# Optimization experiments

Measured on AMD Instinct MI355X. Metric: run time of the kernel, lower is better.

The kernel has to match this reference:

```python
import math
import jax, jax.numpy as jnp
import numpy as np

NH, NKV, HD, THETA = 32, 8, 128, 500000.0

def rotate_half(x):
    x1, x2 = jnp.split(x, 2, axis=-1)
    return jnp.concatenate((-x2, x1), axis=-1)

def rope_cos_sin(seq_len, dim, base, dtype):
    inv_freq = 1.0 / (base ** (jnp.arange(0, dim, 2, dtype=jnp.float32) / dim))
    t = jnp.arange(seq_len, dtype=jnp.float32)
    freqs = jnp.outer(t, inv_freq)              # [S, dim/2]
    emb = jnp.concatenate((freqs, freqs), -1)   # [S, dim]
    return jnp.cos(emb).astype(dtype), jnp.sin(emb).astype(dtype)

def setup_inputs() -> dict:
    key = jax.random.key(0)
    ks = jax.random.split(key, 5)
    B, S, H = 1, 2048, 4096
    sc = 1.0 / math.sqrt(H)
    return {
        'x':  jax.random.normal(ks[0], (B, S, H), jnp.float32),
        'wq': jax.random.normal(ks[1], (H, H), jnp.float32) * sc,
        'wk': jax.random.normal(ks[2], (NKV * HD, H), jnp.float32) * sc,
        'wv': jax.random.normal(ks[3], (NKV * HD, H), jnp.float32) * sc,
        'wo': jax.random.normal(ks[4], (H, H), jnp.float32) * sc,
    }

def attention(x, wq, wk, wv, wo):
    B, S, H = x.shape
    n_rep = NH // NKV
    q = (x @ wq.T).reshape(B, S, NH, HD).transpose(0, 2, 1, 3)    # [B,NH,S,HD]
    k = (x @ wk.T).reshape(B, S, NKV, HD).transpose(0, 2, 1, 3)   # [B,NKV,S,HD]
    v = (x @ wv.T).reshape(B, S, NKV, HD).transpose(0, 2, 1, 3)
    cos, sin = rope_cos_sin(S, HD, THETA, x.dtype)                # [S,HD]
    cos = cos[None, None]; sin = sin[None, None]
    q = q * cos + rotate_half(q) * sin
    k = k * cos + rotate_half(k) * sin
    k = jnp.repeat(k, n_rep, axis=1)                               # [B,NH,S,HD]
    v = jnp.repeat(v, n_rep, axis=1)
    scores = jnp.einsum('bhqd,bhkd->bhqk', q, k) / math.sqrt(HD)
    causal = jnp.tril(jnp.ones((S, S), dtype=bool))
    scores = jnp.where(causal, scores, jnp.finfo(scores.dtype).min)
    probs = jax.nn.softmax(scores, axis=-1)
    out = jnp.einsum('bhqk,bhkd->bhqd', probs, v)                  # [B,NH,S,HD]
    out = out.transpose(0, 2, 1, 3).reshape(B, S, H)
    return out @ wo.T

def reference(x, wq, wk, wv, wo):
    return attention(x, wq, wk, wv, wo)
```

## Files before the change

kernel.cpp:

```cpp
#include <hip/hip_runtime.h>
#include <hip/hip_bf16.h>
#include <math.h>

typedef __bf16 bf16x8 __attribute__((ext_vector_type(8)));
typedef __bf16 bf16x4 __attribute__((ext_vector_type(4)));
typedef unsigned short u16x8 __attribute__((ext_vector_type(8)));
typedef float  f32x4  __attribute__((ext_vector_type(4)));

constexpr int kS   = 2048;
constexpr int kH   = 4096;
constexpr int kNH  = 32;
constexpr int kNKV = 8;
constexpr int kHD  = 128;
constexpr int kQKV = kH + 2 * kNKV * kHD;
constexpr int kKOff = kH;
constexpr int kVOff = kH + kNKV * kHD;

__global__ void cast_bf16(const float* __restrict__ in, __bf16* __restrict__ out, int n4) {
    int i = blockIdx.x * blockDim.x + threadIdx.x;
    if (i < n4) {
        float4 f = ((const float4*)in)[i];
        bf16x4 o;
        o[0] = (__bf16)f.x; o[1] = (__bf16)f.y; o[2] = (__bf16)f.z; o[3] = (__bf16)f.w;
        ((bf16x4*)out)[i] = o;
    }
}

__global__ void cast_all(const float* __restrict__ x, const float* __restrict__ wq,
                         const float* __restrict__ wk, const float* __restrict__ wv,
                         __bf16* __restrict__ xb, __bf16* __restrict__ wqkv) {
    int i = blockIdx.x * 256 + threadIdx.x;
    float4 f;
    __bf16* dst;
    int di;
    if (i < (1 << 21)) {
        f = ((const float4*)x)[i];
        dst = xb; di = i;
    } else {
        int j = i - (1 << 21);
        const float4* s = (j < (1 << 22)) ? ((const float4*)wq + j)
                        : (j < (5 << 20)) ? ((const float4*)wk + (j - (1 << 22)))
                                          : ((const float4*)wv + (j - (5 << 20)));
        f = *s;
        dst = wqkv; di = j;
    }
    bf16x4 o;
    o[0] = (__bf16)f.x; o[1] = (__bf16)f.y; o[2] = (__bf16)f.z; o[3] = (__bf16)f.w;
    ((bf16x4*)dst)[di] = o;
}

constexpr int BM = 128, BN = 128, BK = 64;

__device__ inline void gld16(const __bf16* g, __bf16* l) {
    __builtin_amdgcn_global_load_lds((const __attribute__((address_space(1))) void*)g,
                                     (__attribute__((address_space(3))) void*)l, 16, 0, 0);
}

template <typename OutT>
__global__ __launch_bounds__(256) void gemm_nt(const __bf16* __restrict__ A,
                                               const __bf16* __restrict__ B,
                                               OutT* __restrict__ C,
                                               int M, int N, int K) {
    __shared__ __align__(16) __bf16 As[BM * BK];
    __shared__ __align__(16) __bf16 Bs[BN * BK];
    const int tid  = threadIdx.x;
    const int w    = tid >> 6, lane = tid & 63;
    const int m0   = blockIdx.y * BM, n0 = blockIdx.x * BN;
    const int wm   = (w >> 1) * 64, wn = (w & 1) * 64;
    const int lr   = lane & 15, g8 = lane >> 4;

    const int l3 = lane >> 3;
    const int lc = (lane & 7) ^ l3;
    const __bf16 *gA[4], *gB[4];
    __bf16 *lA[4], *lB[4];
#pragma unroll
    for (int c = 0; c < 4; c++) {
        int G = w * 4 + c;
        gA[c] = A + (size_t)(m0 + G * 8 + l3) * K + lc * 8;
        gB[c] = B + (size_t)(n0 + G * 8 + l3) * K + lc * 8;
        lA[c] = As + G * 512;
        lB[c] = Bs + G * 512;
    }

    f32x4 acc[4][4];
#pragma unroll
    for (int i = 0; i < 4; i++)
#pragma unroll
        for (int j = 0; j < 4; j++) acc[i][j] = (f32x4)(0.f);

    for (int k0 = 0; k0 < K; k0 += BK) {
#pragma unroll
        for (int c = 0; c < 4; c++) {
            gld16(gA[c] + k0, lA[c]);
            gld16(gB[c] + k0, lB[c]);
        }
        __syncthreads();

        const int rx = lr & 7;
#pragma unroll
        for (int kc = 0; kc < 2; kc++) {
            bf16x8 af[4], bfr[4];
#pragma unroll
            for (int i = 0; i < 4; i++)
                af[i]  = *(const bf16x8*)&As[(wm + i * 16 + lr) * BK + (((kc * 4 + g8) ^ rx) * 8)];
#pragma unroll
            for (int j = 0; j < 4; j++)
                bfr[j] = *(const bf16x8*)&Bs[(wn + j * 16 + lr) * BK + (((kc * 4 + g8) ^ rx) * 8)];
#pragma unroll
            for (int i = 0; i < 4; i++)
#pragma unroll
                for (int j = 0; j < 4; j++)
                    acc[i][j] = __builtin_amdgcn_mfma_f32_16x16x32_bf16(af[i], bfr[j], acc[i][j], 0, 0, 0);
        }
        __syncthreads();
    }

    const int cr = g8 * 4, cc = lr;
#pragma unroll
    for (int i = 0; i < 4; i++)
#pragma unroll
        for (int j = 0; j < 4; j++) {
            OutT* Cp = C + (size_t)(m0 + wm + i * 16 + cr) * N + (n0 + wn + j * 16 + cc);
#pragma unroll
            for (int r = 0; r < 4; r++) Cp[(size_t)r * N] = (OutT)acc[i][j][r];
        }
}

__global__ void rope_qkv(__bf16* __restrict__ qkv) {
    int idx  = blockIdx.x * 256 + threadIdx.x;
    int d    = idx & 63;
    int rest = idx >> 6;
    int hh   = rest % (kNH + kNKV);
    int s    = rest / (kNH + kNKV);
    float inv_freq = powf(500000.0f, -(float)d * (1.0f / 64.0f));
    float sn, cs;
    sincosf((float)s * inv_freq, &sn, &cs);
    __bf16* base = qkv + (size_t)s * kQKV + ((hh < kNH) ? hh * kHD : kKOff + (hh - kNH) * kHD);
    float sc = (hh < kNH) ? 0.088388347648318447f : 1.0f;
    float a = (float)base[d], b = (float)base[d + 64];
    base[d]      = (__bf16)((a * cs - b * sn) * sc);
    base[d + 64] = (__bf16)((b * cs + a * sn) * sc);
}

constexpr int KSP = 136;
constexpr int VTP = 72;
constexpr int PSP = 68;

__global__ __launch_bounds__(256) void flash_attn(const __bf16* __restrict__ qkv,
                                                  __bf16* __restrict__ ob) {
    __shared__ __align__(16) __bf16 Ks[64 * KSP];
    __shared__ __align__(16) __bf16 Vt[128 * VTP];
    __shared__ __align__(16) float  Ps[4 * 16 * PSP];

    const int tid  = threadIdx.x;
    const int wave = tid >> 6, lane = tid & 63;
    const int bx   = blockIdx.x;
    const int kvh  = bx & 7;
    const int qt   = 127 - (bx >> 3);
    const int h    = kvh * 4 + wave;
    const int r    = lane & 15, g = lane >> 4;
    const int qglob = qt * 16 + r;

    bf16x8 qfrag[4];
    const __bf16* qrow = qkv + (size_t)(qt * 16 + r) * kQKV + h * kHD + g * 8;
#pragma unroll
    for (int c = 0; c < 4; c++) qfrag[c] = *(const bf16x8*)(qrow + c * 32);

    f32x4 o[8];
#pragma unroll
    for (int dt = 0; dt < 8; dt++) o[dt] = (f32x4)(0.f);
    float mrow = -3.0e38f, lrow = 0.f;
    float* Pw = Ps + wave * 16 * PSP;

    const int nkt = qt / 4 + 1;
    const int krow = tid & 63, kcb = (tid >> 6) * 32;
    const __bf16* kbase = qkv + kKOff + kvh * kHD;
    const __bf16* vbase = qkv + kVOff + kvh * kHD;

    for (int kt = 0; kt < nkt; ++kt) {
        const __bf16* Kg = kbase + (size_t)(kt * 64 + krow) * kQKV + kcb;
        __bf16* Kl = Ks + krow * KSP + kcb;
#pragma unroll
        for (int i = 0; i < 4; i++) *(bf16x8*)(Kl + i * 8) = *(const bf16x8*)(Kg + i * 8);
#pragma unroll
        for (int i = 0; i < 2; i++) {
            int task = tid * 2 + i;
            int p = task & 31, c = task >> 5;
            const __bf16* v0 = vbase + (size_t)(kt * 64 + 2 * p) * kQKV + c * 8;
            u16x8 a = __builtin_bit_cast(u16x8, *(const bf16x8*)v0);
            u16x8 b = __builtin_bit_cast(u16x8, *(const bf16x8*)(v0 + kQKV));
#pragma unroll
            for (int j = 0; j < 8; j++) {
                unsigned int pk = (unsigned int)a[j] | ((unsigned int)b[j] << 16);
                *(unsigned int*)(Vt + (c * 8 + j) * VTP + 2 * p) = pk;
            }
        }
        __syncthreads();

        f32x4 st[4];
#pragma unroll
        for (int t = 0; t < 4; t++) st[t] = (f32x4)(0.f);
#pragma unroll
        for (int c = 0; c < 4; c++) {
#pragma unroll
            for (int t = 0; t < 4; t++) {
                bf16x8 kf = *(const bf16x8*)&Ks[(t * 16 + r) * KSP + c * 32 + g * 8];
                st[t] = __builtin_amdgcn_mfma_f32_16x16x32_bf16(kf, qfrag[c], st[t], 0, 0, 0);
            }
        }

        float mloc = -3.0e38f;
#pragma unroll
        for (int t = 0; t < 4; t++)
#pragma unroll
            for (int reg = 0; reg < 4; reg++) {
                int key = kt * 64 + t * 16 + g * 4 + reg;
                float v = (key <= qglob) ? st[t][reg] : -3.0e38f;
                st[t][reg] = v;
                mloc = fmaxf(mloc, v);
            }
        mloc = fmaxf(mloc, __shfl_xor(mloc, 16));
        mloc = fmaxf(mloc, __shfl_xor(mloc, 32));
        float mnew  = fmaxf(mrow, mloc);
        float alpha = __expf(mrow - mnew);
        mrow = mnew;
        float lsum = 0.f;
#pragma unroll
        for (int t = 0; t < 4; t++)
#pragma unroll
            for (int reg = 0; reg < 4; reg++) {
                float pv = __expf(st[t][reg] - mnew);
                st[t][reg] = pv;
                lsum += pv;
            }
        lsum += __shfl_xor(lsum, 16);
        lsum += __shfl_xor(lsum, 32);
        lrow = lrow * alpha + lsum;

        float ar[4];
#pragma unroll
        for (int reg = 0; reg < 4; reg++) ar[reg] = __shfl(alpha, g * 4 + reg);
#pragma unroll
        for (int dt = 0; dt < 8; dt++)
#pragma unroll
            for (int reg = 0; reg < 4; reg++) o[dt][reg] *= ar[reg];

#pragma unroll
        for (int t = 0; t < 4; t++)
            *(f32x4*)&Pw[r * PSP + t * 16 + g * 4] = st[t];
        __asm__ volatile("s_waitcnt lgkmcnt(0)" ::: "memory");

#pragma unroll
        for (int kc = 0; kc < 2; kc++) {
            f32x4 p0 = *(const f32x4*)&Pw[r * PSP + kc * 32 + g * 8];
            f32x4 p1 = *(const f32x4*)&Pw[r * PSP + kc * 32 + g * 8 + 4];
            bf16x8 pf;
#pragma unroll
            for (int j = 0; j < 4; j++) { pf[j] = (__bf16)p0[j]; pf[j + 4] = (__bf16)p1[j]; }
#pragma unroll
            for (int dt = 0; dt < 8; dt++) {
                bf16x8 vf = *(const bf16x8*)&Vt[(dt * 16 + r) * VTP + kc * 32 + g * 8];
                o[dt] = __builtin_amdgcn_mfma_f32_16x16x32_bf16(pf, vf, o[dt], 0, 0, 0);
            }
        }
        __syncthreads();
    }

    float linv = 1.f / lrow;
    float lr4[4];
#pragma unroll
    for (int reg = 0; reg < 4; reg++) lr4[reg] = __shfl(linv, g * 4 + reg);
#pragma unroll
    for (int dt = 0; dt < 8; dt++)
#pragma unroll
        for (int reg = 0; reg < 4; reg++) {
            int qq = g * 4 + reg, dd = dt * 16 + r;
            ob[(size_t)(qt * 16 + qq) * kH + h * kHD + dd] = (__bf16)(o[dt][reg] * lr4[reg]);
        }
}

extern "C" void kernel_launch(void* const* d_in, const int* in_sizes, int n_in,
                              void* d_out, int out_size, void* d_ws, size_t ws_size,
                              hipStream_t stream) {
    const float* x  = (const float*)d_in[0];
    const float* wq = (const float*)d_in[1];
    const float* wk = (const float*)d_in[2];
    const float* wv = (const float*)d_in[3];
    const float* wo = (const float*)d_in[4];
    float* out = (float*)d_out;

    char* p = (char*)d_ws;
    auto alloc = [&](size_t bytes) {
        char* r = p;
        p += (bytes + 255) & ~(size_t)255;
        return r;
    };
    __bf16* xb    = (__bf16*)alloc((size_t)kS * kH * 2);
    __bf16* wqkvb = (__bf16*)alloc((size_t)kQKV * kH * 2);
    __bf16* qkv   = (__bf16*)alloc((size_t)kS * kQKV * 2);
    __bf16* ao    = xb;
    __bf16* wob   = wqkvb;

    cast_all<<<dim3(1 << 15), 256, 0, stream>>>(x, wq, wk, wv, xb, wqkvb);

    gemm_nt<__bf16><<<dim3(kQKV / BN, kS / BM), 256, 0, stream>>>(xb, wqkvb, qkv, kS, kQKV, kH);

    rope_qkv<<<dim3(kS * (kNH + kNKV) * 64 / 256), 256, 0, stream>>>(qkv);

    cast_bf16<<<dim3((kH * kH / 4) / 256), 256, 0, stream>>>(wo, wob, kH * kH / 4);

    flash_attn<<<dim3(kNKV * (kS / 16)), 256, 0, stream>>>(qkv, ao);

    gemm_nt<float><<<dim3(kH / BN, kS / BM), 256, 0, stream>>>(ao, wob, out, kS, kH, kH);
}
```

Before: 529.0 us.

## Pair causal query tiles per block and load K via direct-to-LDS swizzled copies

Each flash-attention block now handles two query tiles, a long one (127-pi) and a short one (pi), so every block gets an equal causal workload. The grid shrinks from 1024 to 512 blocks. K is loaded through a gld16 helper (apparently a direct global-to-LDS load) into an unpadded XOR-swizzled layout, masking runs only on the last key tile, and P is staged in LDS as bf16 rather than fp32. The aim is to remove tail imbalance, padding and mask overhead and to halve P traffic, at the cost of fewer blocks and serial tile processing inside each block.

```diff
diff --git a/kernel.cpp b/kernel.cpp
--- a/kernel.cpp
+++ b/kernel.cpp
@@ -142,141 +142,155 @@
     base[d + 64] = (__bf16)((b * cs + a * sn) * sc);
 }
 
-constexpr int KSP = 136;
 constexpr int VTP = 72;
-constexpr int PSP = 68;
+constexpr int PSB = 72;
 
 __global__ __launch_bounds__(256) void flash_attn(const __bf16* __restrict__ qkv,
                                                   __bf16* __restrict__ ob) {
-    __shared__ __align__(16) __bf16 Ks[64 * KSP];
+    __shared__ __align__(16) __bf16 Ks[64 * 128];
     __shared__ __align__(16) __bf16 Vt[128 * VTP];
-    __shared__ __align__(16) float  Ps[4 * 16 * PSP];
+    __shared__ __align__(16) __bf16 Ps[4 * 16 * PSB];
 
     const int tid  = threadIdx.x;
     const int wave = tid >> 6, lane = tid & 63;
     const int bx   = blockIdx.x;
     const int kvh  = bx & 7;
-    const int qt   = 127 - (bx >> 3);
+    const int pi   = bx >> 3;
     const int h    = kvh * 4 + wave;
     const int r    = lane & 15, g = lane >> 4;
-    const int qglob = qt * 16 + r;
-
-    bf16x8 qfrag[4];
-    const __bf16* qrow = qkv + (size_t)(qt * 16 + r) * kQKV + h * kHD + g * 8;
-#pragma unroll
-    for (int c = 0; c < 4; c++) qfrag[c] = *(const bf16x8*)(qrow + c * 32);
-
-    f32x4 o[8];
-#pragma unroll
-    for (int dt = 0; dt < 8; dt++) o[dt] = (f32x4)(0.f);
-    float mrow = -3.0e38f, lrow = 0.f;
-    float* Pw = Ps + wave * 16 * PSP;
-
-    const int nkt = qt / 4 + 1;
-    const int krow = tid & 63, kcb = (tid >> 6) * 32;
+
+    __bf16* Pw = Ps + wave * 16 * PSB;
     const __bf16* kbase = qkv + kKOff + kvh * kHD;
     const __bf16* vbase = qkv + kVOff + kvh * kHD;
 
-    for (int kt = 0; kt < nkt; ++kt) {
-        const __bf16* Kg = kbase + (size_t)(kt * 64 + krow) * kQKV + kcb;
-        __bf16* Kl = Ks + krow * KSP + kcb;
-#pragma unroll
-        for (int i = 0; i < 4; i++) *(bf16x8*)(Kl + i * 8) = *(const bf16x8*)(Kg + i * 8);
-#pragma unroll
-        for (int i = 0; i < 2; i++) {
-            int task = tid * 2 + i;
-            int p = task & 31, c = task >> 5;
-            const __bf16* v0 = vbase + (size_t)(kt * 64 + 2 * p) * kQKV + c * 8;
-            u16x8 a = __builtin_bit_cast(u16x8, *(const bf16x8*)v0);
-            u16x8 b = __builtin_bit_cast(u16x8, *(const bf16x8*)(v0 + kQKV));
-#pragma unroll
-            for (int j = 0; j < 8; j++) {
-                unsigned int pk = (unsigned int)a[j] | ((unsigned int)b[j] << 16);
-                *(unsigned int*)(Vt + (c * 8 + j) * VTP + 2 * p) = pk;
-            }
+    int krow[4], kgc[4];
+#pragma unroll
+    for (int c = 0; c < 4; c++) {
+        krow[c] = wave * 16 + c * 4 + (lane >> 4);
+        kgc[c]  = (lane & 15) ^ (krow[c] & 15);
+    }
+
+    for (int qp = 0; qp < 2; qp++) {
+        const int qt = qp ? pi : 127 - pi;
+        const int qglob = qt * 16 + r;
+
+        bf16x8 qfrag[4];
+        const __bf16* qrow = qkv + (size_t)(qt * 16 + r) * kQKV + h * kHD + g * 8;
+#pragma unroll
+        for (int c = 0; c < 4; c++) qfrag[c] = *(const bf16x8*)(qrow + c * 32);
+
+        f32x4 o[8];
+#pragma unroll
+        for (int dt = 0; dt < 8; dt++) o[dt] = (f32x4)(0.f);
+        float mrow = -3.0e38f, lrow = 0.f;
+
+        const int nkt = qt / 4 + 1;
+        for (int kt = 0; kt < nkt; ++kt) {
+#pragma unroll
+            for (int c = 0; c < 4; c++)
+                gld16(kbase + (size_t)(kt * 64 + krow[c]) * kQKV + kgc[c] * 8,
+                      Ks + (wave * 4 + c) * 512);
+#pragma unroll
+            for (int i = 0; i < 2; i++) {
+                int task = i * 256 + tid;
+                int p = task & 31, c = task >> 5;
+                const __bf16* v0 = vbase + (size_t)(kt * 64 + 2 * p) * kQKV + c * 8;
+                u16x8 a = __builtin_bit_cast(u16x8, *(const bf16x8*)v0);
+                u16x8 b = __builtin_bit_cast(u16x8, *(const bf16x8*)(v0 + kQKV));
+#pragma unroll
+                for (int j = 0; j < 8; j++) {
+                    unsigned int pk = (unsigned int)a[j] | ((unsigned int)b[j] << 16);
+                    *(unsigned int*)(Vt + (c * 8 + j) * VTP + 2 * p) = pk;
+                }
+            }
+            __syncthreads();
+
+            f32x4 st[4];
+#pragma unroll
+            for (int t = 0; t < 4; t++) st[t] = (f32x4)(0.f);
+#pragma unroll
+            for (int c = 0; c < 4; c++) {
+#pragma unroll
+                for (int t = 0; t < 4; t++) {
+                    bf16x8 kf = *(const bf16x8*)&Ks[(t * 16 + r) * 128 + (((c * 4 + g) ^ r) * 8)];
+                    st[t] = __builtin_amdgcn_mfma_f32_16x16x32_bf16(kf, qfrag[c], st[t], 0, 0, 0);
+                }
+            }
+
+            if (kt == nkt - 1) {
+#pragma unroll
+                for (int t = 0; t < 4; t++)
+#pragma unroll
+                    for (int reg = 0; reg < 4; reg++) {
+                        int key = kt * 64 + t * 16 + g * 4 + reg;
+                        if (key > qglob) st[t][reg] = -3.0e38f;
+                    }
+            }
+
+            float mloc = -3.0e38f;
+#pragma unroll
+            for (int t = 0; t < 4; t++)
+#pragma unroll
+                for (int reg = 0; reg < 4; reg++) mloc = fmaxf(mloc, st[t][reg]);
+            mloc = fmaxf(mloc, __shfl_xor(mloc, 16));
+            mloc = fmaxf(mloc, __shfl_xor(mloc, 32));
+            float mnew  = fmaxf(mrow, mloc);
+            float alpha = __expf(mrow - mnew);
+            mrow = mnew;
+            float lsum = 0.f;
+#pragma unroll
+            for (int t = 0; t < 4; t++)
+#pragma unroll
+                for (int reg = 0; reg < 4; reg++) {
+                    float pv = __expf(st[t][reg] - mnew);
+                    st[t][reg] = pv;
+                    lsum += pv;
+                }
+            lsum += __shfl_xor(lsum, 16);
+            lsum += __shfl_xor(lsum, 32);
+            lrow = lrow * alpha + lsum;
+
+            float ar[4];
+#pragma unroll
+            for (int reg = 0; reg < 4; reg++) ar[reg] = __shfl(alpha, g * 4 + reg);
+#pragma unroll
+            for (int dt = 0; dt < 8; dt++)
+#pragma unroll
+                for (int reg = 0; reg < 4; reg++) o[dt][reg] *= ar[reg];
+
+#pragma unroll
+            for (int t = 0; t < 4; t++) {
+                bf16x4 pb;
+#pragma unroll
+                for (int j = 0; j < 4; j++) pb[j] = (__bf16)st[t][j];
+                *(bf16x4*)&Pw[r * PSB + t * 16 + g * 4] = pb;
+            }
+            __asm__ volatile("s_waitcnt lgkmcnt(0)" ::: "memory");
+
+#pragma unroll
+            for (int kc = 0; kc < 2; kc++) {
+                bf16x8 pf = *(const bf16x8*)&Pw[r * PSB + kc * 32 + g * 8];
+#pragma unroll
+                for (int dt = 0; dt < 8; dt++) {
+                    bf16x8 vf = *(const bf16x8*)&Vt[(dt * 16 + r) * VTP + kc * 32 + g * 8];
+                    o[dt] = __builtin_amdgcn_mfma_f32_16x16x32_bf16(pf, vf, o[dt], 0, 0, 0);
+                }
+            }
+            __syncthreads();
         }
-        __syncthreads();
-
-        f32x4 st[4];
-#pragma unroll
-        for (int t = 0; t < 4; t++) st[t] = (f32x4)(0.f);
-#pragma unroll
-        for (int c = 0; c < 4; c++) {
-#pragma unroll
-            for (int t = 0; t < 4; t++) {
-                bf16x8 kf = *(const bf16x8*)&Ks[(t * 16 + r) * KSP + c * 32 + g * 8];
-                st[t] = __builtin_amdgcn_mfma_f32_16x16x32_bf16(kf, qfrag[c], st[t], 0, 0, 0);
-            }
-        }
-
-        float mloc = -3.0e38f;
-#pragma unroll
-        for (int t = 0; t < 4; t++)
+
+        float linv = 1.f / lrow;
+        float lr4[4];
+#pragma unroll
+        for (int reg = 0; reg < 4; reg++) lr4[reg] = __shfl(linv, g * 4 + reg);
+#pragma unroll
+        for (int dt = 0; dt < 8; dt++)
 #pragma unroll
             for (int reg = 0; reg < 4; reg++) {
-                int key = kt * 64 + t * 16 + g * 4 + reg;
-                float v = (key <= qglob) ? st[t][reg] : -3.0e38f;
-                st[t][reg] = v;
-                mloc = fmaxf(mloc, v);
-            }
-        mloc = fmaxf(mloc, __shfl_xor(mloc, 16));
-        mloc = fmaxf(mloc, __shfl_xor(mloc, 32));
-        float mnew  = fmaxf(mrow, mloc);
-        float alpha = __expf(mrow - mnew);
-        mrow = mnew;
-        float lsum = 0.f;
-#pragma unroll
-        for (int t = 0; t < 4; t++)
-#pragma unroll
-            for (int reg = 0; reg < 4; reg++) {
-                float pv = __expf(st[t][reg] - mnew);
-                st[t][reg] = pv;
-                lsum += pv;
-            }
-        lsum += __shfl_xor(lsum, 16);
-        lsum += __shfl_xor(lsum, 32);
-        lrow = lrow * alpha + lsum;
-
-        float ar[4];
-#pragma unroll
-        for (int reg = 0; reg < 4; reg++) ar[reg] = __shfl(alpha, g * 4 + reg);
-#pragma unroll
-        for (int dt = 0; dt < 8; dt++)
-#pragma unroll
-            for (int reg = 0; reg < 4; reg++) o[dt][reg] *= ar[reg];
-
-#pragma unroll
-        for (int t = 0; t < 4; t++)
-            *(f32x4*)&Pw[r * PSP + t * 16 + g * 4] = st[t];
-        __asm__ volatile("s_waitcnt lgkmcnt(0)" ::: "memory");
-
-#pragma unroll
-        for (int kc = 0; kc < 2; kc++) {
-            f32x4 p0 = *(const f32x4*)&Pw[r * PSP + kc * 32 + g * 8];
-            f32x4 p1 = *(const f32x4*)&Pw[r * PSP + kc * 32 + g * 8 + 4];
-            bf16x8 pf;
-#pragma unroll
-            for (int j = 0; j < 4; j++) { pf[j] = (__bf16)p0[j]; pf[j + 4] = (__bf16)p1[j]; }
-#pragma unroll
-            for (int dt = 0; dt < 8; dt++) {
-                bf16x8 vf = *(const bf16x8*)&Vt[(dt * 16 + r) * VTP + kc * 32 + g * 8];
-                o[dt] = __builtin_amdgcn_mfma_f32_16x16x32_bf16(pf, vf, o[dt], 0, 0, 0);
-            }
-        }
-        __syncthreads();
-    }
-
-    float linv = 1.f / lrow;
-    float lr4[4];
-#pragma unroll
-    for (int reg = 0; reg < 4; reg++) lr4[reg] = __shfl(linv, g * 4 + reg);
-#pragma unroll
-    for (int dt = 0; dt < 8; dt++)
-#pragma unroll
-        for (int reg = 0; reg < 4; reg++) {
-            int qq = g * 4 + reg, dd = dt * 16 + r;
-            ob[(size_t)(qt * 16 + qq) * kH + h * kHD + dd] = (__bf16)(o[dt][reg] * lr4[reg]);
-        }
+                int qq = g * 4 + reg, dd = dt * 16 + r;
+                ob[(size_t)(qt * 16 + qq) * kH + h * kHD + dd] = (__bf16)(o[dt][reg] * lr4[reg]);
+            }
+    }
 }
 
 extern "C" void kernel_launch(void* const* d_in, const int* in_sizes, int n_in,
@@ -309,7 +323,7 @@
 
     cast_bf16<<<dim3((kH * kH / 4) / 256), 256, 0, stream>>>(wo, wob, kH * kH / 4);
 
-    flash_attn<<<dim3(kNKV * (kS / 16)), 256, 0, stream>>>(qkv, ao);
+    flash_attn<<<dim3(kNKV * 64), 256, 0, stream>>>(qkv, ao);
 
     gemm_nt<float><<<dim3(kH / BN, kS / BM), 256, 0, stream>>>(ao, wob, out, kS, kH, kH);
 }
```

After: 557.7 us. +5.4%, slower.
